# Optimization experiments

Measured on AMD Instinct MI355X. Metric: run time of the kernel, lower is better.

The kernel has to match this reference:

```python
import jax, jax.numpy as jnp
import numpy as np

N, E, F_IN, F_OUT, PERIODS = 40000, 640000, 64, 128, 12


def setup_inputs() -> dict:
    key = jax.random.key(0)
    ks = jax.random.split(key, 24)
    def w(k, shape):
        return jax.random.normal(k, shape, jnp.float32) * 0.05
    inp = {
        "X": jax.random.normal(ks[0], (N, F_IN, PERIODS), jnp.float32),
        "edge_index": jax.random.randint(ks[1], (2, E), 0, N),
        "edge_weight": jax.random.uniform(ks[2], (E,), jnp.float32),
        "attention": jax.random.uniform(ks[3], (PERIODS,), jnp.float32),
    }
    for idx, g in enumerate(["i", "f", "c", "o"]):
        inp[f"W_x{g}"] = w(ks[4 + 4 * idx], (F_IN, F_OUT))
        inp[f"b_x{g}"] = jnp.zeros((F_OUT,), jnp.float32)
        inp[f"W_h{g}"] = w(ks[5 + 4 * idx], (2 * F_OUT, F_OUT))
        inp[f"b_h{g}"] = jnp.zeros((F_OUT,), jnp.float32)
    return inp


def reference(X, edge_index, edge_weight, attention,
              W_xi, b_xi, W_hi, b_hi,
              W_xf, b_xf, W_hf, b_hf,
              W_xc, b_xc, W_hc, b_hc,
              W_xo, b_xo, W_ho, b_ho):
    n = X.shape[0]
    # GCN normalization with self-loops: D^-1/2 (A + I) D^-1/2
    loops = jnp.arange(n)
    rows = jnp.concatenate([edge_index[0], loops])  # sources
    cols = jnp.concatenate([edge_index[1], loops])  # targets
    wts = jnp.concatenate([edge_weight, jnp.ones((n,), X.dtype)])
    deg = jax.ops.segment_sum(wts, cols, num_segments=n)
    dinv = jnp.where(deg > 0, jax.lax.rsqrt(deg), 0.0)
    norm = dinv[rows] * wts * dinv[cols]  # [E+N]

    def gcn(x, W, b):
        xw = x @ W  # [N, F_OUT]
        agg = jax.ops.segment_sum(norm[:, None] * xw[rows], cols, num_segments=n)
        return agg + b

    probs = jax.nn.softmax(attention)
    H0 = jnp.zeros((n, W_hi.shape[1]), X.dtype)
    C0 = jnp.zeros_like(H0)
    Xp = jnp.moveaxis(X, 2, 0)  # [periods, N, F_IN]

    def step(carry, xs):
        H, C, Hacc = carry
        x_t, p = xs
        def gate(Wx, bx, Wh, bh):
            return jnp.concatenate([gcn(x_t, Wx, bx), H], axis=1) @ Wh + bh
        I = jax.nn.sigmoid(gate(W_xi, b_xi, W_hi, b_hi))
        F = jax.nn.sigmoid(gate(W_xf, b_xf, W_hf, b_hf))
        Ct = jnp.tanh(gate(W_xc, b_xc, W_hc, b_hc))
        O = jax.nn.sigmoid(gate(W_xo, b_xo, W_ho, b_ho))
        C_new = F * C + I * Ct
        H_new = O * jnp.tanh(C_new)
        return (H_new, C_new, Hacc + p * H_new), None

    (H, C, Hacc), _ = jax.lax.scan(step, (H0, C0, H0), (Xp, probs))
    return Hacc
```

## Files before the change

### kernel.cpp

```cpp
#include <hip/hip_runtime.h>

typedef __bf16 bf16_t;
typedef bf16_t bf16x4 __attribute__((ext_vector_type(4)));
typedef bf16_t bf16x8 __attribute__((ext_vector_type(8)));
typedef float floatx4 __attribute__((ext_vector_type(4)));

#define F_INq 64
#define F_OUTq 128
#define PERIODSq 12
#define XROW (F_INq * PERIODSq)

__global__ __launch_bounds__(256) void k_init(float* deg, int* counts, int N) {
  int i = blockIdx.x * 256 + threadIdx.x;
  if (i < N) { deg[i] = 1.0f; counts[i] = 0; }
}

__global__ __launch_bounds__(256) void k_accum(const int* __restrict__ ei, const float* __restrict__ ew,
                                               float* deg, int* counts, int E) {
  int e = blockIdx.x * 256 + threadIdx.x;
  if (e < E) {
    int c = ei[E + e];
    atomicAdd(&deg[c], ew[e]);
    atomicAdd(&counts[c], 1);
  }
}

__global__ __launch_bounds__(256) void k_dinv(float* deg, int N) {
  int i = blockIdx.x * 256 + threadIdx.x;
  if (i < N) { float d = deg[i]; deg[i] = d > 0.0f ? rsqrtf(d) : 0.0f; }
}

__global__ __launch_bounds__(256) void k_scanA(const int* __restrict__ counts, int* __restrict__ bsum, int N) {
  __shared__ int ws[4];
  int b = blockIdx.x, t = threadIdx.x;
  int base = b * 1024 + t * 4;
  int s = 0;
  if (base + 3 < N) {
    int4 c = *(const int4*)(counts + base);
    s = c.x + c.y + c.z + c.w;
  } else {
    for (int k = 0; k < 4; ++k) if (base + k < N) s += counts[base + k];
  }
  for (int off = 1; off < 64; off <<= 1) s += __shfl_xor(s, off);
  int lane = t & 63, w = t >> 6;
  if (lane == 0) ws[w] = s;
  __syncthreads();
  if (t == 0) bsum[b] = ws[0] + ws[1] + ws[2] + ws[3];
}

__global__ __launch_bounds__(64) void k_scanB(const int* __restrict__ bsum, int* __restrict__ bbase, int nb) {
  int t = threadIdx.x;
  int v = t < nb ? bsum[t] : 0;
  int inc = v;
  for (int off = 1; off < 64; off <<= 1) {
    int u = __shfl_up(inc, off);
    if (t >= off) inc += u;
  }
  if (t < nb) bbase[t] = inc - v;
  if (t == nb - 1) bbase[nb] = inc;
}

__global__ __launch_bounds__(256) void k_scanC(const int* __restrict__ counts, const int* __restrict__ bbase,
                                               int* __restrict__ offs, int* __restrict__ cursor, int N, int nb) {
  __shared__ int ws[4];
  int b = blockIdx.x, t = threadIdx.x;
  int base = b * 1024 + t * 4;
  int c0_ = 0, c1_ = 0, c2_ = 0, c3_ = 0;
  if (base + 3 < N) {
    int4 c = *(const int4*)(counts + base);
    c0_ = c.x; c1_ = c.y; c2_ = c.z; c3_ = c.w;
  } else {
    if (base < N) c0_ = counts[base];
    if (base + 1 < N) c1_ = counts[base + 1];
    if (base + 2 < N) c2_ = counts[base + 2];
    if (base + 3 < N) c3_ = counts[base + 3];
  }
  int tot = c0_ + c1_ + c2_ + c3_;
  int lane = t & 63, w = t >> 6;
  int inc = tot;
  for (int off = 1; off < 64; off <<= 1) {
    int u = __shfl_up(inc, off);
    if (lane >= off) inc += u;
  }
  if (lane == 63) ws[w] = inc;
  __syncthreads();
  int wb = bbase[b];
  for (int i = 0; i < w; ++i) wb += ws[i];
  int e = wb + inc - tot;
  if (base < N)     { offs[base] = e;                 cursor[base] = e; }
  if (base + 1 < N) { int o = e + c0_;                offs[base + 1] = o; cursor[base + 1] = o; }
  if (base + 2 < N) { int o = e + c0_ + c1_;          offs[base + 2] = o; cursor[base + 2] = o; }
  if (base + 3 < N) { int o = e + c0_ + c1_ + c2_;    offs[base + 3] = o; cursor[base + 3] = o; }
  if (b == 0 && t == 0) offs[N] = bbase[nb];
}

__global__ __launch_bounds__(1024) void k_scan(const int* __restrict__ counts, int* __restrict__ offs,
                                               int* __restrict__ cursor, int N) {
  __shared__ int sd[1024];
  int t = threadIdx.x;
  int CH = (N + 1023) >> 10;
  int base = t * CH;
  int sum = 0;
  for (int i = 0; i < CH; ++i) { int idx = base + i; if (idx < N) sum += counts[idx]; }
  sd[t] = sum;
  __syncthreads();
  for (int off = 1; off < 1024; off <<= 1) {
    int v = (t >= off) ? sd[t - off] : 0;
    __syncthreads();
    sd[t] += v;
    __syncthreads();
  }
  int run = sd[t] - sum;
  for (int i = 0; i < CH; ++i) {
    int idx = base + i;
    if (idx < N) { offs[idx] = run; cursor[idx] = run; run += counts[idx]; }
  }
  if (t == 1023) offs[N] = sd[1023];
}

__global__ __launch_bounds__(256) void k_scatter(const int* __restrict__ ei, const float* __restrict__ ew,
                                                 const float* __restrict__ dinv, int* cursor,
                                                 int* __restrict__ csr_src, float* __restrict__ csr_nrm, int E) {
  int e = blockIdx.x * 256 + threadIdx.x;
  if (e < E) {
    int r = ei[e], c = ei[E + e];
    int p = atomicAdd(&cursor[c], 1);
    csr_src[p] = r;
    csr_nrm[p] = dinv[r] * ew[e] * dinv[c];
  }
}

__global__ __launch_bounds__(256) void k_prew(
    const float* __restrict__ Wxi, const float* __restrict__ Whi,
    const float* __restrict__ Wxf, const float* __restrict__ Whf,
    const float* __restrict__ Wxc, const float* __restrict__ Whc,
    const float* __restrict__ Wxo, const float* __restrict__ Who,
    const float* __restrict__ bxi, const float* __restrict__ bhi,
    const float* __restrict__ bxf, const float* __restrict__ bhf,
    const float* __restrict__ bxc, const float* __restrict__ bhc,
    const float* __restrict__ bxo, const float* __restrict__ bho,
    const float* __restrict__ att,
    bf16_t* __restrict__ WbT, float* __restrict__ bcomb, float* __restrict__ probs) {
  const int WT = 512 * 192;
  int gid = blockIdx.x * 256 + threadIdx.x;
  if (gid < WT) {
    int col = gid / 192, k = gid % 192;
    int g = col >> 7, j = col & 127;
    const float* Wx = g == 0 ? Wxi : g == 1 ? Wxf : g == 2 ? Wxc : Wxo;
    const float* Wh = g == 0 ? Whi : g == 1 ? Whf : g == 2 ? Whc : Who;
    float s;
    if (k < 64) {
      s = 0.0f;
      for (int kk = 0; kk < 128; ++kk) s += Wx[k * 128 + kk] * Wh[kk * 128 + j];
    } else {
      s = Wh[(k + 64) * 128 + j];
    }
    WbT[(size_t)col * 192 + k] = (bf16_t)s;
  } else if (gid < WT + 512) {
    int cc = gid - WT;
    int g = cc >> 7, j = cc & 127;
    const float* bx = g == 0 ? bxi : g == 1 ? bxf : g == 2 ? bxc : bxo;
    const float* bh = g == 0 ? bhi : g == 1 ? bhf : g == 2 ? bhc : bho;
    const float* Wh = g == 0 ? Whi : g == 1 ? Whf : g == 2 ? Whc : Who;
    float s = bh[j];
    for (int kk = 0; kk < 128; ++kk) s += bx[kk] * Wh[kk * 128 + j];
    bcomb[cc] = s;
  } else if (gid == WT + 512) {
    float m = att[0];
    for (int i = 1; i < PERIODSq; ++i) m = fmaxf(m, att[i]);
    float e[PERIODSq], s = 0.0f;
    for (int i = 0; i < PERIODSq; ++i) { e[i] = __expf(att[i] - m); s += e[i]; }
    for (int i = 0; i < PERIODSq; ++i) probs[i] = e[i] / s;
  }
}

__global__ __launch_bounds__(192) void k_xpose(const float* __restrict__ X, bf16_t* __restrict__ Xb) {
  __shared__ float lds[XROW];
  const int n = blockIdx.x, tid = threadIdx.x;
  const float4* Xr = (const float4*)(X + (size_t)n * XROW);
  float4 v = Xr[tid];
  lds[tid * 4 + 0] = v.x;
  lds[tid * 4 + 1] = v.y;
  lds[tid * 4 + 2] = v.z;
  lds[tid * 4 + 3] = v.w;
  __syncthreads();
  const int o = tid * 4;
  bf16x4 r;
#pragma unroll
  for (int k = 0; k < 4; ++k) {
    int oo = o + k;
    int tt = oo >> 6, f = oo & 63;
    r[k] = (bf16_t)lds[f * PERIODSq + tt];
  }
  *(bf16x4*)(Xb + (size_t)n * XROW + o) = r;
}

__global__ __launch_bounds__(256) void k_agg2(const bf16_t* __restrict__ Xb, const int* __restrict__ csr_src,
                                              const float* __restrict__ csr_nrm, const int* __restrict__ offs,
                                              const float* __restrict__ dinv, bf16_t* __restrict__ Xagg, int N) {
  const int node = blockIdx.x * 4 + (threadIdx.x >> 6);
  const int lane = threadIdx.x & 63;
  const int s0 = offs[node], s1 = offs[node + 1];
  floatx4 a0 = {0.f, 0.f, 0.f, 0.f}, a1 = a0, a2 = a0;
  int e = s0;
  for (; e + 8 <= s1; e += 8) {
    bf16x4 v[8][3];
    float nn[8];
#pragma unroll
    for (int u = 0; u < 8; ++u) {
      int s = csr_src[e + u];
      nn[u] = csr_nrm[e + u];
      const bf16x4* xp = (const bf16x4*)(Xb + (size_t)s * XROW) + lane;
      v[u][0] = xp[0]; v[u][1] = xp[64]; v[u][2] = xp[128];
    }
#pragma unroll
    for (int u = 0; u < 8; ++u) {
#pragma unroll
      for (int k = 0; k < 4; ++k) {
        a0[k] += nn[u] * (float)v[u][0][k];
        a1[k] += nn[u] * (float)v[u][1][k];
        a2[k] += nn[u] * (float)v[u][2][k];
      }
    }
  }
  for (; e < s1; ++e) {
    int s = csr_src[e];
    float nr = csr_nrm[e];
    const bf16x4* xp = (const bf16x4*)(Xb + (size_t)s * XROW) + lane;
    bf16x4 v0 = xp[0], v1 = xp[64], v2 = xp[128];
#pragma unroll
    for (int k = 0; k < 4; ++k) {
      a0[k] += nr * (float)v0[k];
      a1[k] += nr * (float)v1[k];
      a2[k] += nr * (float)v2[k];
    }
  }
  float dc = dinv[node];
  float self = dc * dc;
  const bf16x4* xc = (const bf16x4*)(Xb + (size_t)node * XROW) + lane;
  {
    bf16x4 v0 = xc[0], v1 = xc[64], v2 = xc[128];
#pragma unroll
    for (int k = 0; k < 4; ++k) {
      a0[k] += self * (float)v0[k];
      a1[k] += self * (float)v1[k];
      a2[k] += self * (float)v2[k];
    }
  }
  const int f4 = lane & 15, tq = lane >> 4;
  floatx4 accs[3] = {a0, a1, a2};
#pragma unroll
  for (int j = 0; j < 3; ++j) {
    int tt = tq + 4 * j;
    bf16x4 r;
#pragma unroll
    for (int k = 0; k < 4; ++k) r[k] = (bf16_t)accs[j][k];
    *(bf16x4*)(Xagg + ((size_t)tt * N + node) * 64 + f4 * 4) = r;
  }
}

__global__ __launch_bounds__(256) void k_agg(const float* __restrict__ X, const int* __restrict__ csr_src,
                                             const float* __restrict__ csr_nrm, const int* __restrict__ offs,
                                             const float* __restrict__ dinv, bf16_t* __restrict__ Xagg, int N) {
  int c = blockIdx.x;
  int tid = threadIdx.x;
  int s0 = offs[c], s1 = offs[c + 1];
  const int i0 = tid, i1 = tid + 256, i2 = tid + 512;
  float a0 = 0.f, a1 = 0.f, a2 = 0.f;
  for (int e = s0; e < s1; ++e) {
    int s = csr_src[e];
    float nr = csr_nrm[e];
    const float* xp = X + (size_t)s * XROW;
    a0 += nr * xp[i0]; a1 += nr * xp[i1]; a2 += nr * xp[i2];
  }
  float dc = dinv[c];
  float self = dc * dc;
  const float* xc = X + (size_t)c * XROW;
  a0 += self * xc[i0]; a1 += self * xc[i1]; a2 += self * xc[i2];
  __shared__ float lds[XROW];
  lds[i0] = a0; lds[i1] = a1; lds[i2] = a2;
  __syncthreads();
  for (int o = tid; o < XROW; o += 256) {
    int tt = o >> 6, f = o & 63;
    Xagg[(size_t)tt * N * 64 + (size_t)c * 64 + f] = (bf16_t)lds[f * PERIODSq + tt];
  }
}

__global__ __launch_bounds__(512, 2) void k_gate_all(const bf16_t* __restrict__ Xagg,
                                                     const bf16_t* __restrict__ WbT,
                                                     const float* __restrict__ bcomb,
                                                     const float* __restrict__ probs,
                                                     float* __restrict__ out, int N) {
  __shared__ __align__(16) char Hs[2][32 * 256];
  const int tid = threadIdx.x;
  const int lane = tid & 63, w = tid >> 6;
  const int q = lane >> 4, c0 = lane & 15;
  const int n0 = blockIdx.x * 32;
  const int swz = c0 & 7;

  bf16x8 Wf[4][6];
#pragma unroll
  for (int g = 0; g < 4; ++g) {
    const bf16_t* wp = WbT + (size_t)((g * 8 + w) * 16 + c0) * 192;
#pragma unroll
    for (int ks = 0; ks < 6; ++ks) Wf[g][ks] = *(const bf16x8*)(wp + ks * 32 + q * 8);
  }
  floatx4 bv[4];
#pragma unroll
  for (int g = 0; g < 4; ++g) bv[g] = *(const floatx4*)(bcomb + g * 128 + w * 16 + q * 4);

  floatx4 Cst[2], Ha[2];
#pragma unroll
  for (int rt = 0; rt < 2; ++rt) {
    Cst[rt] = (floatx4){0.f, 0.f, 0.f, 0.f};
    Ha[rt] = (floatx4){0.f, 0.f, 0.f, 0.f};
  }

  const bf16_t* Xrow0 = Xagg + (size_t)(n0 + c0) * 64 + q * 8;
  const bf16_t* Xrow1 = Xagg + (size_t)(n0 + 16 + c0) * 64 + q * 8;

  bf16x8 Xf0 = *(const bf16x8*)(Xrow0);
  bf16x8 Xf1 = *(const bf16x8*)(Xrow0 + 32);
  bf16x8 Xf2 = *(const bf16x8*)(Xrow1);
  bf16x8 Xf3 = *(const bf16x8*)(Xrow1 + 32);

  floatx4 accA[2][4], accB[2][4];
#pragma unroll
  for (int g = 0; g < 4; ++g) { accA[0][g] = bv[g]; accA[1][g] = bv[g]; }
#pragma unroll
  for (int g = 0; g < 4; ++g) {
    accA[0][g] = __builtin_amdgcn_mfma_f32_16x16x32_bf16(Wf[g][0], Xf0, accA[0][g], 0, 0, 0);
    accA[0][g] = __builtin_amdgcn_mfma_f32_16x16x32_bf16(Wf[g][1], Xf1, accA[0][g], 0, 0, 0);
    accA[1][g] = __builtin_amdgcn_mfma_f32_16x16x32_bf16(Wf[g][0], Xf2, accA[1][g], 0, 0, 0);
    accA[1][g] = __builtin_amdgcn_mfma_f32_16x16x32_bf16(Wf[g][1], Xf3, accA[1][g], 0, 0, 0);
  }

  const float NL2E = -1.44269504f;
  const float T2L2E = 2.88539008f;

#define PERIOD(T, AC, AN, RB, WB, DO_H, DO_NEXT)                                                      \
  do {                                                                                                \
    if (DO_NEXT) {                                                                                    \
      const size_t toff_ = (size_t)((T) + 1) * N * 64;                                                \
      Xf0 = *(const bf16x8*)(Xrow0 + toff_);                                                          \
      Xf1 = *(const bf16x8*)(Xrow0 + toff_ + 32);                                                     \
      Xf2 = *(const bf16x8*)(Xrow1 + toff_);                                                          \
      Xf3 = *(const bf16x8*)(Xrow1 + toff_ + 32);                                                     \
    }                                                                                                 \
    if (DO_H) {                                                                                       \
      _Pragma("unroll") for (int ks = 0; ks < 4; ++ks) {                                              \
        bf16x8 B0 = *(const bf16x8*)(&Hs[RB][(c0) * 256 + (((4 * ks + q) ^ swz) << 4)]);              \
        bf16x8 B1 = *(const bf16x8*)(&Hs[RB][(16 + c0) * 256 + (((4 * ks + q) ^ swz) << 4)]);         \
        _Pragma("unroll") for (int g = 0; g < 4; ++g) {                                               \
          AC[0][g] = __builtin_amdgcn_mfma_f32_16x16x32_bf16(Wf[g][ks + 2], B0, AC[0][g], 0, 0, 0);   \
          AC[1][g] = __builtin_amdgcn_mfma_f32_16x16x32_bf16(Wf[g][ks + 2], B1, AC[1][g], 0, 0, 0);   \
        }                                                                                             \
      }                                                                                               \
    }                                                                                                 \
    const float pt_ = probs[T];                                                                       \
    _Pragma("unroll") for (int rt = 0; rt < 2; ++rt) {                                                \
      bf16x4 hv_;                                                                                     \
      _Pragma("unroll") for (int r = 0; r < 4; ++r) {                                                 \
        float pI = AC[rt][0][r], pF = AC[rt][1][r], pC = AC[rt][2][r], pO = AC[rt][3][r];             \
        float I_ = __builtin_amdgcn_rcpf(1.0f + __builtin_amdgcn_exp2f(pI * NL2E));                   \
        float F_ = __builtin_amdgcn_rcpf(1.0f + __builtin_amdgcn_exp2f(pF * NL2E));                   \
        float Ct_ = fmaf(-2.0f, __builtin_amdgcn_rcpf(1.0f + __builtin_amdgcn_exp2f(pC * T2L2E)), 1.0f); \
        float O_ = __builtin_amdgcn_rcpf(1.0f + __builtin_amdgcn_exp2f(pO * NL2E));                   \
        float Cn_ = fmaf(F_, Cst[rt][r], I_ * Ct_);                                                   \
        Cst[rt][r] = Cn_;                                                                             \
        float tC_ = fmaf(-2.0f, __builtin_amdgcn_rcpf(1.0f + __builtin_amdgcn_exp2f(Cn_ * T2L2E)), 1.0f); \
        float Hn_ = O_ * tC_;                                                                         \
        Ha[rt][r] = fmaf(pt_, Hn_, Ha[rt][r]);                                                        \
        hv_[r] = (bf16_t)Hn_;                                                                         \
      }                                                                                               \
      *(bf16x4*)(&Hs[WB][(rt * 16 + c0) * 256 + (((2 * w + (q >> 1)) ^ swz) << 4) + ((q & 1) * 8)]) = hv_; \
    }                                                                                                 \
    if (DO_NEXT) {                                                                                    \
      _Pragma("unroll") for (int g = 0; g < 4; ++g) { AN[0][g] = bv[g]; AN[1][g] = bv[g]; }           \
      _Pragma("unroll") for (int g = 0; g < 4; ++g) {                                                 \
        AN[0][g] = __builtin_amdgcn_mfma_f32_16x16x32_bf16(Wf[g][0], Xf0, AN[0][g], 0, 0, 0);         \
        AN[0][g] = __builtin_amdgcn_mfma_f32_16x16x32_bf16(Wf[g][1], Xf1, AN[0][g], 0, 0, 0);         \
        AN[1][g] = __builtin_amdgcn_mfma_f32_16x16x32_bf16(Wf[g][0], Xf2, AN[1][g], 0, 0, 0);         \
        AN[1][g] = __builtin_amdgcn_mfma_f32_16x16x32_bf16(Wf[g][1], Xf3, AN[1][g], 0, 0, 0);         \
      }                                                                                               \
    }                                                                                                 \
    __syncthreads();                                                                                  \
  } while (0)

  PERIOD(0, accA, accB, 1, 0, 0, 1);
  for (int tt = 1; tt <= 9; tt += 2) {
    PERIOD(tt, accB, accA, 0, 1, 1, 1);
    PERIOD(tt + 1, accA, accB, 1, 0, 1, 1);
  }
  PERIOD(11, accB, accA, 0, 1, 1, 0);
#undef PERIOD

#pragma unroll
  for (int rt = 0; rt < 2; ++rt) {
    int row = n0 + rt * 16 + c0;
    *(floatx4*)(out + (size_t)row * 128 + w * 16 + q * 4) = Ha[rt];
  }
}

extern "C" void kernel_launch(void* const* d_in, const int* in_sizes, int n_in,
                              void* d_out, int out_size, void* d_ws, size_t ws_size,
                              hipStream_t stream) {
  const float* X = (const float*)d_in[0];
  const int* ei = (const int*)d_in[1];
  const float* ew = (const float*)d_in[2];
  const float* att = (const float*)d_in[3];
  const float* Wxi = (const float*)d_in[4];
  const float* bxi = (const float*)d_in[5];
  const float* Whi = (const float*)d_in[6];
  const float* bhi = (const float*)d_in[7];
  const float* Wxf = (const float*)d_in[8];
  const float* bxf = (const float*)d_in[9];
  const float* Whf = (const float*)d_in[10];
  const float* bhf = (const float*)d_in[11];
  const float* Wxc = (const float*)d_in[12];
  const float* bxc = (const float*)d_in[13];
  const float* Whc = (const float*)d_in[14];
  const float* bhc = (const float*)d_in[15];
  const float* Wxo = (const float*)d_in[16];
  const float* bxo = (const float*)d_in[17];
  const float* Who = (const float*)d_in[18];
  const float* bho = (const float*)d_in[19];
  float* out = (float*)d_out;

  const int N = in_sizes[0] / XROW;
  const int E = in_sizes[2];

  char* base = (char*)d_ws;
  size_t off = 0;
  auto carve = [&](size_t bytes) {
    char* r = base + off;
    off += (bytes + 255) & ~(size_t)255;
    return (void*)r;
  };
  float* deg = (float*)carve((size_t)N * 4);
  int* counts = (int*)carve((size_t)N * 4);
  int* offs = (int*)carve((size_t)(N + 1) * 4);
  int* cursor = (int*)carve((size_t)(N + 1) * 4);
  int* csr_src = (int*)carve((size_t)E * 4);
  float* csr_nrm = (float*)carve((size_t)E * 4);
  bf16_t* WbT = (bf16_t*)carve((size_t)512 * 192 * 2);
  float* bcomb = (float*)carve(512 * 4);
  float* probs = (float*)carve(64);
  int* bsum = (int*)carve(64 * 4);
  int* bbase = (int*)carve(68 * 4);
  bf16_t* Xagg = (bf16_t*)carve((size_t)PERIODSq * N * 64 * 2);
  bf16_t* Xb = (bf16_t*)carve((size_t)N * XROW * 2);
  const bool use_bf16 = (off <= ws_size);

  k_init<<<(N + 255) / 256, 256, 0, stream>>>(deg, counts, N);
  k_accum<<<(E + 255) / 256, 256, 0, stream>>>(ei, ew, deg, counts, E);
  k_dinv<<<(N + 255) / 256, 256, 0, stream>>>(deg, N);
  const int nb = (N + 1023) >> 10;
  if (nb <= 64) {
    k_scanA<<<nb, 256, 0, stream>>>(counts, bsum, N);
    k_scanB<<<1, 64, 0, stream>>>(bsum, bbase, nb);
    k_scanC<<<nb, 256, 0, stream>>>(counts, bbase, offs, cursor, N, nb);
  } else {
    k_scan<<<1, 1024, 0, stream>>>(counts, offs, cursor, N);
  }
  k_scatter<<<(E + 255) / 256, 256, 0, stream>>>(ei, ew, deg, cursor, csr_src, csr_nrm, E);
  k_prew<<<(512 * 192 + 512 + 1 + 255) / 256, 256, 0, stream>>>(
      Wxi, Whi, Wxf, Whf, Wxc, Whc, Wxo, Who,
      bxi, bhi, bxf, bhf, bxc, bhc, bxo, bho, att, WbT, bcomb, probs);

  if (use_bf16) {
    k_xpose<<<N, 192, 0, stream>>>(X, Xb);
    k_agg2<<<N / 4, 256, 0, stream>>>(Xb, csr_src, csr_nrm, offs, deg, Xagg, N);
  } else {
    k_agg<<<N, 256, 0, stream>>>(X, csr_src, csr_nrm, offs, deg, Xagg, N);
  }

  k_gate_all<<<N / 32, 512, 0, stream>>>(Xagg, WbT, bcomb, probs, out, N);
}
```

Baseline: 604.5 us.

## Merge scatter, weight precompute and X transpose into one launch; fold scan stages

Fuses the dinv computation into the first scan pass and drops the separate block-prefix kernel by having each scan block sum the preceding block totals itself. The CSR scatter, weight/bias precompute and X transpose run as block ranges of a single kernel, which removes several launch gaps and lets the independent work overlap. Small gate-kernel tweaks preload the softmax probabilities into registers and feed the bias straight into the first MFMA as its accumulator. The cost is a wider 256-thread block for the transpose role, which leaves 64 threads idle, and a serial bsum loop in each scan block.

Measured after the change: 612.0 us. About the same (+1.2%).

```diff
diff --git a/kernel.cpp b/kernel.cpp
--- a/kernel.cpp
+++ b/kernel.cpp
@@ -30,7 +30,8 @@
   if (i < N) { float d = deg[i]; deg[i] = d > 0.0f ? rsqrtf(d) : 0.0f; }
 }
 
-__global__ __launch_bounds__(256) void k_scanA(const int* __restrict__ counts, int* __restrict__ bsum, int N) {
+__global__ __launch_bounds__(256) void k_scanA(const int* __restrict__ counts, float* __restrict__ deg,
+                                               int* __restrict__ bsum, int N) {
   __shared__ int ws[4];
   int b = blockIdx.x, t = threadIdx.x;
   int base = b * 1024 + t * 4;
@@ -41,6 +42,11 @@
   } else {
     for (int k = 0; k < 4; ++k) if (base + k < N) s += counts[base + k];
   }
+#pragma unroll
+  for (int k = 0; k < 4; ++k) {
+    int idx = base + k;
+    if (idx < N) { float d = deg[idx]; deg[idx] = d > 0.0f ? rsqrtf(d) : 0.0f; }
+  }
   for (int off = 1; off < 64; off <<= 1) s += __shfl_xor(s, off);
   int lane = t & 63, w = t >> 6;
   if (lane == 0) ws[w] = s;
@@ -48,19 +54,7 @@
   if (t == 0) bsum[b] = ws[0] + ws[1] + ws[2] + ws[3];
 }
 
-__global__ __launch_bounds__(64) void k_scanB(const int* __restrict__ bsum, int* __restrict__ bbase, int nb) {
-  int t = threadIdx.x;
-  int v = t < nb ? bsum[t] : 0;
-  int inc = v;
-  for (int off = 1; off < 64; off <<= 1) {
-    int u = __shfl_up(inc, off);
-    if (t >= off) inc += u;
-  }
-  if (t < nb) bbase[t] = inc - v;
-  if (t == nb - 1) bbase[nb] = inc;
-}
-
-__global__ __launch_bounds__(256) void k_scanC(const int* __restrict__ counts, const int* __restrict__ bbase,
+__global__ __launch_bounds__(256) void k_scanC(const int* __restrict__ counts, const int* __restrict__ bsum,
                                                int* __restrict__ offs, int* __restrict__ cursor, int N, int nb) {
   __shared__ int ws[4];
   int b = blockIdx.x, t = threadIdx.x;
@@ -84,14 +78,19 @@
   }
   if (lane == 63) ws[w] = inc;
   __syncthreads();
-  int wb = bbase[b];
+  int wb = 0;
+  for (int i = 0; i < b; ++i) wb += bsum[i];
   for (int i = 0; i < w; ++i) wb += ws[i];
   int e = wb + inc - tot;
   if (base < N)     { offs[base] = e;                 cursor[base] = e; }
   if (base + 1 < N) { int o = e + c0_;                offs[base + 1] = o; cursor[base + 1] = o; }
   if (base + 2 < N) { int o = e + c0_ + c1_;          offs[base + 2] = o; cursor[base + 2] = o; }
   if (base + 3 < N) { int o = e + c0_ + c1_ + c2_;    offs[base + 3] = o; cursor[base + 3] = o; }
-  if (b == 0 && t == 0) offs[N] = bbase[nb];
+  if (b == nb - 1 && t == 0) {
+    int tt2 = 0;
+    for (int i = 0; i < nb - 1; ++i) tt2 += bsum[i];
+    offs[N] = tt2 + ws[0] + ws[1] + ws[2] + ws[3];
+  }
 }
 
 __global__ __launch_bounds__(1024) void k_scan(const int* __restrict__ counts, int* __restrict__ offs,
@@ -174,6 +173,90 @@
   }
 }
 
+__global__ __launch_bounds__(256) void k_mid(
+    const int* __restrict__ ei, const float* __restrict__ ew, const float* __restrict__ dinv,
+    int* cursor, int* __restrict__ csr_src, float* __restrict__ csr_nrm, int E,
+    const float* __restrict__ Wxi, const float* __restrict__ Whi,
+    const float* __restrict__ Wxf, const float* __restrict__ Whf,
+    const float* __restrict__ Wxc, const float* __restrict__ Whc,
+    const float* __restrict__ Wxo, const float* __restrict__ Who,
+    const float* __restrict__ bxi, const float* __restrict__ bhi,
+    const float* __restrict__ bxf, const float* __restrict__ bhf,
+    const float* __restrict__ bxc, const float* __restrict__ bhc,
+    const float* __restrict__ bxo, const float* __restrict__ bho,
+    const float* __restrict__ att,
+    bf16_t* __restrict__ WbT, float* __restrict__ bcomb, float* __restrict__ probs,
+    const float* __restrict__ X, bf16_t* __restrict__ Xb,
+    int nbScatter, int nbPrew) {
+  __shared__ float lds[XROW];
+  const int b = blockIdx.x, tid = threadIdx.x;
+  if (b < nbScatter) {
+    int e = b * 256 + tid;
+    if (e < E) {
+      int r = ei[e], c = ei[E + e];
+      int p = atomicAdd(&cursor[c], 1);
+      csr_src[p] = r;
+      csr_nrm[p] = dinv[r] * ew[e] * dinv[c];
+    }
+    return;
+  }
+  if (b < nbScatter + nbPrew) {
+    const int WT = 512 * 192;
+    int gid = (b - nbScatter) * 256 + tid;
+    if (gid < WT) {
+      int col = gid / 192, k = gid % 192;
+      int g = col >> 7, j = col & 127;
+      const float* Wx = g == 0 ? Wxi : g == 1 ? Wxf : g == 2 ? Wxc : Wxo;
+      const float* Wh = g == 0 ? Whi : g == 1 ? Whf : g == 2 ? Whc : Who;
+      float s;
+      if (k < 64) {
+        s = 0.0f;
+        for (int kk = 0; kk < 128; ++kk) s += Wx[k * 128 + kk] * Wh[kk * 128 + j];
+      } else {
+        s = Wh[(k + 64) * 128 + j];
+      }
+      WbT[(size_t)col * 192 + k] = (bf16_t)s;
+    } else if (gid < WT + 512) {
+      int cc = gid - WT;
+      int g = cc >> 7, j = cc & 127;
+      const float* bx = g == 0 ? bxi : g == 1 ? bxf : g == 2 ? bxc : bxo;
+      const float* bh = g == 0 ? bhi : g == 1 ? bhf : g == 2 ? bhc : bho;
+      const float* Wh = g == 0 ? Whi : g == 1 ? Whf : g == 2 ? Whc : Who;
+      float s = bh[j];
+      for (int kk = 0; kk < 128; ++kk) s += bx[kk] * Wh[kk * 128 + j];
+      bcomb[cc] = s;
+    } else if (gid == WT + 512) {
+      float m = att[0];
+      for (int i = 1; i < PERIODSq; ++i) m = fmaxf(m, att[i]);
+      float e[PERIODSq], s = 0.0f;
+      for (int i = 0; i < PERIODSq; ++i) { e[i] = __expf(att[i] - m); s += e[i]; }
+      for (int i = 0; i < PERIODSq; ++i) probs[i] = e[i] / s;
+    }
+    return;
+  }
+  const int n = b - nbScatter - nbPrew;
+  if (tid < 192) {
+    const float4* Xr = (const float4*)(X + (size_t)n * XROW);
+    float4 v = Xr[tid];
+    lds[tid * 4 + 0] = v.x;
+    lds[tid * 4 + 1] = v.y;
+    lds[tid * 4 + 2] = v.z;
+    lds[tid * 4 + 3] = v.w;
+  }
+  __syncthreads();
+  if (tid < 192) {
+    const int o = tid * 4;
+    bf16x4 r;
+#pragma unroll
+    for (int k = 0; k < 4; ++k) {
+      int oo = o + k;
+      int tt = oo >> 6, f = oo & 63;
+      r[k] = (bf16_t)lds[f * PERIODSq + tt];
+    }
+    *(bf16x4*)(Xb + (size_t)n * XROW + o) = r;
+  }
+}
+
 __global__ __launch_bounds__(192) void k_xpose(const float* __restrict__ X, bf16_t* __restrict__ Xb) {
   __shared__ float lds[XROW];
   const int n = blockIdx.x, tid = threadIdx.x;
@@ -308,6 +391,9 @@
   floatx4 bv[4];
 #pragma unroll
   for (int g = 0; g < 4; ++g) bv[g] = *(const floatx4*)(bcomb + g * 128 + w * 16 + q * 4);
+  float pr[PERIODSq];
+#pragma unroll
+  for (int i = 0; i < PERIODSq; ++i) pr[i] = probs[i];
 
   floatx4 Cst[2], Ha[2];
 #pragma unroll
@@ -326,12 +412,10 @@
 
   floatx4 accA[2][4], accB[2][4];
 #pragma unroll
-  for (int g = 0; g < 4; ++g) { accA[0][g] = bv[g]; accA[1][g] = bv[g]; }
-#pragma unroll
   for (int g = 0; g < 4; ++g) {
-    accA[0][g] = __builtin_amdgcn_mfma_f32_16x16x32_bf16(Wf[g][0], Xf0, accA[0][g], 0, 0, 0);
+    accA[0][g] = __builtin_amdgcn_mfma_f32_16x16x32_bf16(Wf[g][0], Xf0, bv[g], 0, 0, 0);
     accA[0][g] = __builtin_amdgcn_mfma_f32_16x16x32_bf16(Wf[g][1], Xf1, accA[0][g], 0, 0, 0);
-    accA[1][g] = __builtin_amdgcn_mfma_f32_16x16x32_bf16(Wf[g][0], Xf2, accA[1][g], 0, 0, 0);
+    accA[1][g] = __builtin_amdgcn_mfma_f32_16x16x32_bf16(Wf[g][0], Xf2, bv[g], 0, 0, 0);
     accA[1][g] = __builtin_amdgcn_mfma_f32_16x16x32_bf16(Wf[g][1], Xf3, accA[1][g], 0, 0, 0);
   }
 
@@ -357,7 +441,7 @@
         }                                                                                             \
       }                                                                                               \
     }                                                                                                 \
-    const float pt_ = probs[T];                                                                       \
+    const float pt_ = pr[T];                                                                          \
     _Pragma("unroll") for (int rt = 0; rt < 2; ++rt) {                                                \
       bf16x4 hv_;                                                                                     \
       _Pragma("unroll") for (int r = 0; r < 4; ++r) {                                                 \
@@ -376,11 +460,10 @@
       *(bf16x4*)(&Hs[WB][(rt * 16 + c0) * 256 + (((2 * w + (q >> 1)) ^ swz) << 4) + ((q & 1) * 8)]) = hv_; \
     }                                                                                                 \
     if (DO_NEXT) {                                                                                    \
-      _Pragma("unroll") for (int g = 0; g < 4; ++g) { AN[0][g] = bv[g]; AN[1][g] = bv[g]; }           \
       _Pragma("unroll") for (int g = 0; g < 4; ++g) {                                                 \
-        AN[0][g] = __builtin_amdgcn_mfma_f32_16x16x32_bf16(Wf[g][0], Xf0, AN[0][g], 0, 0, 0);         \
+        AN[0][g] = __builtin_amdgcn_mfma_f32_16x16x32_bf16(Wf[g][0], Xf0, bv[g], 0, 0, 0);            \
         AN[0][g] = __builtin_amdgcn_mfma_f32_16x16x32_bf16(Wf[g][1], Xf1, AN[0][g], 0, 0, 0);         \
-        AN[1][g] = __builtin_amdgcn_mfma_f32_16x16x32_bf16(Wf[g][0], Xf2, AN[1][g], 0, 0, 0);         \
+        AN[1][g] = __builtin_amdgcn_mfma_f32_16x16x32_bf16(Wf[g][0], Xf2, bv[g], 0, 0, 0);            \
         AN[1][g] = __builtin_amdgcn_mfma_f32_16x16x32_bf16(Wf[g][1], Xf3, AN[1][g], 0, 0, 0);         \
       }                                                                                               \
     }                                                                                                 \
@@ -447,31 +530,35 @@
   float* bcomb = (float*)carve(512 * 4);
   float* probs = (float*)carve(64);
   int* bsum = (int*)carve(64 * 4);
-  int* bbase = (int*)carve(68 * 4);
   bf16_t* Xagg = (bf16_t*)carve((size_t)PERIODSq * N * 64 * 2);
   bf16_t* Xb = (bf16_t*)carve((size_t)N * XROW * 2);
-  const bool use_bf16 = (off <= ws_size);
+  const bool use_bf16 = (off <= ws_size) && ((N & 3) == 0);
 
   k_init<<<(N + 255) / 256, 256, 0, stream>>>(deg, counts, N);
   k_accum<<<(E + 255) / 256, 256, 0, stream>>>(ei, ew, deg, counts, E);
-  k_dinv<<<(N + 255) / 256, 256, 0, stream>>>(deg, N);
   const int nb = (N + 1023) >> 10;
   if (nb <= 64) {
-    k_scanA<<<nb, 256, 0, stream>>>(counts, bsum, N);
-    k_scanB<<<1, 64, 0, stream>>>(bsum, bbase, nb);
-    k_scanC<<<nb, 256, 0, stream>>>(counts, bbase, offs, cursor, N, nb);
+    k_scanA<<<nb, 256, 0, stream>>>(counts, deg, bsum, N);
+    k_scanC<<<nb, 256, 0, stream>>>(counts, bsum, offs, cursor, N, nb);
   } else {
+    k_dinv<<<(N + 255) / 256, 256, 0, stream>>>(deg, N);
     k_scan<<<1, 1024, 0, stream>>>(counts, offs, cursor, N);
   }
-  k_scatter<<<(E + 255) / 256, 256, 0, stream>>>(ei, ew, deg, cursor, csr_src, csr_nrm, E);
-  k_prew<<<(512 * 192 + 512 + 1 + 255) / 256, 256, 0, stream>>>(
-      Wxi, Whi, Wxf, Whf, Wxc, Whc, Wxo, Who,
-      bxi, bhi, bxf, bhf, bxc, bhc, bxo, bho, att, WbT, bcomb, probs);
-
+
+  const int nbScatter = (E + 255) / 256;
+  const int nbPrew = (512 * 192 + 512 + 1 + 255) / 256;
   if (use_bf16) {
-    k_xpose<<<N, 192, 0, stream>>>(X, Xb);
+    k_mid<<<nbScatter + nbPrew + N, 256, 0, stream>>>(
+        ei, ew, deg, cursor, csr_src, csr_nrm, E,
+        Wxi, Whi, Wxf, Whf, Wxc, Whc, Wxo, Who,
+        bxi, bhi, bxf, bhf, bxc, bhc, bxo, bho, att, WbT, bcomb, probs,
+        X, Xb, nbScatter, nbPrew);
     k_agg2<<<N / 4, 256, 0, stream>>>(Xb, csr_src, csr_nrm, offs, deg, Xagg, N);
   } else {
+    k_scatter<<<nbScatter, 256, 0, stream>>>(ei, ew, deg, cursor, csr_src, csr_nrm, E);
+    k_prew<<<nbPrew, 256, 0, stream>>>(
+        Wxi, Whi, Wxf, Whf, Wxc, Whc, Wxo, Who,
+        bxi, bhi, bxf, bhf, bxc, bhc, bxo, bho, att, WbT, bcomb, probs);
     k_agg<<<N, 256, 0, stream>>>(X, csr_src, csr_nrm, offs, deg, Xagg, N);
   }
 
```
